# Optimization experiments

Hardware: AMD Instinct MI355X
Metric: run time of the kernel (lower is better)

## Reference

```python
import jax, jax.numpy as jnp
import numpy as np

TOP_K = 5


def setup_inputs() -> dict:
    key = jax.random.key(0)
    k1, k2 = jax.random.split(key)
    batch, n_attr, feat_dim = 4096, 64000, 512  # 1000 classes x 64 attrs
    image_features = jax.random.normal(k1, (batch, feat_dim), dtype=jnp.float32)
    # raw (unnormalized) attribute concept features, flattened to (n_attr, feat_dim)
    attr_features = jax.random.normal(k2, (n_attr, feat_dim), dtype=jnp.float32)
    return {"image_features": image_features, "attr_features": attr_features}


def reference(image_features, attr_features):
    # __init__: L2-normalize attribute features along feature dim
    attr_norm = attr_features / jnp.linalg.norm(attr_features, axis=-1, keepdims=True)
    # similarities: (batch, n_attr) dense dot-product matrix
    similarities = image_features @ attr_norm.T
    # top-k along attribute dim
    top_scores, top_indices = jax.lax.top_k(similarities, TOP_K)
    # gather selected attribute vectors: (batch, top_k, feat_dim)
    top_attr_features = attr_norm[top_indices]
    return (top_attr_features, top_scores)
```

## Files before the change

### kernel.cpp

```cpp
#include <hip/hip_runtime.h>
#include <float.h>

#define FEAT 512
#define TOPK 5
#define NSEL 16
#define BM 256
#define BN 256
#define BKT 64
#define NKT (FEAT / BKT)
#define ABYTES (BM * BKT)
#define BUFB (2 * ABYTES)
#define NCB 4

typedef __attribute__((ext_vector_type(4))) int i32x4;

__device__ __forceinline__ void gl_lds16(const void* g, void* lds) {
    __builtin_amdgcn_global_load_lds(
        (const __attribute__((address_space(1))) unsigned int*)g,
        (__attribute__((address_space(3))) unsigned int*)lds, 16, 0, 0);
}

__global__ __launch_bounds__(256) void quant_attr(
    const float* __restrict__ in, signed char* __restrict__ q,
    float* __restrict__ inv) {
    const int w = threadIdx.x >> 6, l = threadIdx.x & 63;
    const int row = blockIdx.x * 4 + w;
    const float4* p = reinterpret_cast<const float4*>(in) + (size_t)row * (FEAT / 4);
    const float4 v0 = p[l * 2], v1 = p[l * 2 + 1];
    float ss = v0.x * v0.x + v0.y * v0.y + v0.z * v0.z + v0.w * v0.w +
               v1.x * v1.x + v1.y * v1.y + v1.z * v1.z + v1.w * v1.w;
#pragma unroll
    for (int m = 1; m < 64; m <<= 1) ss += __shfl_xor(ss, m);
    const float iv = 1.0f / sqrtf(fmaxf(ss, 1e-30f));
    const float qs = iv * 300.0f;
    int qv[8];
    qv[0] = __float2int_rn(v0.x * qs); qv[1] = __float2int_rn(v0.y * qs);
    qv[2] = __float2int_rn(v0.z * qs); qv[3] = __float2int_rn(v0.w * qs);
    qv[4] = __float2int_rn(v1.x * qs); qv[5] = __float2int_rn(v1.y * qs);
    qv[6] = __float2int_rn(v1.z * qs); qv[7] = __float2int_rn(v1.w * qs);
#pragma unroll
    for (int j = 0; j < 8; ++j) qv[j] = min(127, max(-127, qv[j]));
    int2 st;
    st.x = (qv[0] & 255) | ((qv[1] & 255) << 8) | ((qv[2] & 255) << 16) |
           ((unsigned)(qv[3] & 255) << 24);
    st.y = (qv[4] & 255) | ((qv[5] & 255) << 8) | ((qv[6] & 255) << 16) |
           ((unsigned)(qv[7] & 255) << 24);
    *reinterpret_cast<int2*>(q + (size_t)row * FEAT + l * 8) = st;
    if (l == 0) inv[row] = iv;
}

__global__ __launch_bounds__(256) void quant_img(
    const float* __restrict__ in, signed char* __restrict__ q) {
    const int w = threadIdx.x >> 6, l = threadIdx.x & 63;
    const int row = blockIdx.x * 4 + w;
    const float4* p = reinterpret_cast<const float4*>(in) + (size_t)row * (FEAT / 4);
    const float4 v0 = p[l * 2], v1 = p[l * 2 + 1];
    float mx = fmaxf(fmaxf(fmaxf(fabsf(v0.x), fabsf(v0.y)), fmaxf(fabsf(v0.z), fabsf(v0.w))),
                     fmaxf(fmaxf(fabsf(v1.x), fabsf(v1.y)), fmaxf(fabsf(v1.z), fabsf(v1.w))));
#pragma unroll
    for (int m = 1; m < 64; m <<= 1) mx = fmaxf(mx, __shfl_xor(mx, m));
    mx = fmaxf(mx, 1e-20f);
    const float qs = 127.0f / mx;
    const int q0 = __float2int_rn(v0.x * qs), q1 = __float2int_rn(v0.y * qs);
    const int q2 = __float2int_rn(v0.z * qs), q3 = __float2int_rn(v0.w * qs);
    const int q4 = __float2int_rn(v1.x * qs), q5 = __float2int_rn(v1.y * qs);
    const int q6 = __float2int_rn(v1.z * qs), q7 = __float2int_rn(v1.w * qs);
    int2 st;
    st.x = (q0 & 255) | ((q1 & 255) << 8) | ((q2 & 255) << 16) | ((unsigned)(q3 & 255) << 24);
    st.y = (q4 & 255) | ((q5 & 255) << 8) | ((q6 & 255) << 16) | ((unsigned)(q7 & 255) << 24);
    *reinterpret_cast<int2*>(q + (size_t)row * FEAT + l * 8) = st;
}

__global__ __launch_bounds__(512, 2) void coarse_kernel(
    const signed char* __restrict__ attrQ, const signed char* __restrict__ imgQ,
    unsigned* __restrict__ cand, int nablk, int niblk) {
    __shared__ __align__(1024) char lds[3][BUFB];
    const int tid = threadIdx.x;

    const int cpx = gridDim.x >> 3;
    const int wg = ((int)blockIdx.x & 7) * cpx + ((int)blockIdx.x >> 3);
    const int ablock = wg / niblk;
    const int iblock = wg % niblk;

    const int w = tid >> 6, l = tid & 63;
    const int wr = w >> 2, wc = w & 3;
    const int lrow = l & 15, lg = l >> 4;

    const int srow = tid >> 2, sg = tid & 3;
    const int ssw = sg ^ ((srow ^ (srow >> 2)) & 3);
    const signed char* asrc = attrQ + (size_t)(ablock * BM + srow) * FEAT + (ssw << 4);
    const signed char* bsrc = imgQ + (size_t)(iblock * BN + srow) * FEAT + (ssw << 4);

    int a_off[8], b_off[4];
#pragma unroll
    for (int m = 0; m < 8; ++m) {
        const int r = wr * 128 + m * 16 + lrow;
        a_off[m] = r * BKT + ((lg ^ ((r ^ (r >> 2)) & 3)) << 4);
    }
#pragma unroll
    for (int n = 0; n < 4; ++n) {
        const int r = wc * 64 + n * 16 + lrow;
        b_off[n] = ABYTES + r * BKT + ((lg ^ ((r ^ (r >> 2)) & 3)) << 4);
    }

    i32x4 acc[8][4];
#pragma unroll
    for (int m = 0; m < 8; ++m)
#pragma unroll
        for (int n = 0; n < 4; ++n) acc[m][n] = (i32x4){0, 0, 0, 0};

#define STAGE(bufi, kt)                                                      \
    {                                                                        \
        char* d_ = &lds[bufi][tid * 16];                                     \
        gl_lds16(asrc + (kt) * BKT, d_);                                     \
        gl_lds16(asrc + (kt) * BKT + (size_t)128 * FEAT, d_ + 8192);         \
        gl_lds16(bsrc + (kt) * BKT, d_ + 16384);                             \
        gl_lds16(bsrc + (kt) * BKT + (size_t)128 * FEAT, d_ + 24576);        \
    }

    STAGE(0, 0);
    int cur = 0, nxt = 1;
#pragma unroll 1
    for (int t = 0; t < NKT; ++t) {
        if (t < NKT - 1) {
            STAGE(nxt, t + 1);
            asm volatile("s_waitcnt vmcnt(4)" ::: "memory");
        } else {
            asm volatile("s_waitcnt vmcnt(0)" ::: "memory");
        }
        __builtin_amdgcn_s_barrier();
        __builtin_amdgcn_sched_barrier(0);
        const char* buf = &lds[cur][0];
        i32x4 bF[4], aF[8];
#pragma unroll
        for (int n = 0; n < 4; ++n)
            bF[n] = *reinterpret_cast<const i32x4*>(buf + b_off[n]);
#pragma unroll
        for (int m = 0; m < 8; ++m)
            aF[m] = *reinterpret_cast<const i32x4*>(buf + a_off[m]);
        __builtin_amdgcn_s_setprio(1);
#pragma unroll
        for (int m = 0; m < 8; ++m)
#pragma unroll
            for (int n = 0; n < 4; ++n)
                acc[m][n] = __builtin_amdgcn_mfma_i32_16x16x64_i8(
                    aF[m], bF[n], acc[m][n], 0, 0, 0);
        __builtin_amdgcn_s_setprio(0);
        cur = (cur == 2) ? 0 : cur + 1;
        nxt = (nxt == 2) ? 0 : nxt + 1;
    }
#undef STAGE

    unsigned m1[4] = {0u, 0u, 0u, 0u}, m2[4] = {0u, 0u, 0u, 0u};
#pragma unroll
    for (int m = 0; m < 8; ++m)
#pragma unroll
        for (int r = 0; r < 4; ++r) {
            const int rowl = wr * 128 + m * 16 + lg * 4 + r;
            const unsigned idxc = 2047u - (unsigned)rowl;
#pragma unroll
            for (int n = 0; n < 4; ++n) {
                const unsigned p =
                    (((unsigned)(acc[m][n][r] + (1 << 23)) << 8) & 0xFFFFF800u) | idxc;
                m2[n] = max(m2[n], min(m1[n], p));
                m1[n] = max(m1[n], p);
            }
        }

    unsigned* scratch = reinterpret_cast<unsigned*>(&lds[0][0]);
#pragma unroll
    for (int n = 0; n < 4; ++n) {
        scratch[(w * 64 + l) * 8 + n * 2] = m1[n];
        scratch[(w * 64 + l) * 8 + n * 2 + 1] = m2[n];
    }
    __syncthreads();

    if (tid < BN) {
        const int wc2 = tid >> 6, cw = tid & 63;
        const int n = cw >> 4, lr = cw & 15;
        unsigned best[NCB] = {0u, 0u, 0u, 0u};
#pragma unroll
        for (int wr2 = 0; wr2 < 2; ++wr2)
#pragma unroll
            for (int lg2 = 0; lg2 < 4; ++lg2)
#pragma unroll
                for (int k = 0; k < 2; ++k) {
                    const unsigned p =
                        scratch[((wr2 * 4 + wc2) * 64 + lg2 * 16 + lr) * 8 + n * 2 + k];
                    if (p > best[NCB - 1]) {
                        best[NCB - 1] = p;
#pragma unroll
                        for (int x = NCB - 1; x > 0; --x)
                            if (best[x] > best[x - 1]) {
                                const unsigned t_ = best[x];
                                best[x] = best[x - 1]; best[x - 1] = t_;
                            }
                    }
                }
        const size_t base = ((size_t)(iblock * BN + tid) * nablk + ablock) * NCB;
#pragma unroll
        for (int j = 0; j < NCB; ++j) cand[base + j] = best[j];
    }
}

__global__ __launch_bounds__(64) void select16_kernel(
    const unsigned* __restrict__ cand, int* __restrict__ sel, int nablk) {
    const int row = blockIdx.x;
    const int l = threadIdx.x;
    const int ncand = nablk * NCB;
    const unsigned* cr = cand + (size_t)row * ncand;
    unsigned p[16]; int c[16];
#pragma unroll
    for (int j = 0; j < 16; ++j) {
        const int slot = l * 16 + j;
        if (slot < ncand) {
            const unsigned v = cr[slot];
            p[j] = v;
            c[j] = (slot / NCB) * BM + (2047 - (int)(v & 0x7FFu));
        } else { p[j] = 0u; c[j] = 0x7fffffff; }
    }
    int* out = sel + (size_t)row * NSEL;
    for (int r = 0; r < NSEL; ++r) {
        unsigned bp = 0u; int bc = 0x7fffffff;
#pragma unroll
        for (int j = 0; j < 16; ++j)
            if (p[j] > bp || (p[j] == bp && c[j] < bc)) { bp = p[j]; bc = c[j]; }
#pragma unroll
        for (int m = 1; m < 64; m <<= 1) {
            const unsigned op = __shfl_xor(bp, m);
            const int oc = __shfl_xor(bc, m);
            if (op > bp || (op == bp && oc < bc)) { bp = op; bc = oc; }
        }
        if (l == 0) out[r] = bc;
#pragma unroll
        for (int j = 0; j < 16; ++j)
            if (p[j] == bp && c[j] == bc) { p[j] = 0u; c[j] = 0x7fffffff; }
    }
}

__global__ __launch_bounds__(256) void rescore_kernel(
    const float* __restrict__ img, const float* __restrict__ attr,
    const float* __restrict__ inv, const int* __restrict__ sel,
    float* __restrict__ out_scores, int* __restrict__ final_i) {
    __shared__ float s_sc[NSEL];
    const int row = blockIdx.x;
    const int w = threadIdx.x >> 6, l = threadIdx.x & 63;
    const float4* ip = reinterpret_cast<const float4*>(img) + (size_t)row * (FEAT / 4);
    const float4 a0 = ip[l * 2], a1 = ip[l * 2 + 1];
#pragma unroll
    for (int q = 0; q < 4; ++q) {
        const int slot = w * 4 + q;
        const int ci = sel[(size_t)row * NSEL + slot];
        const float4* ap = reinterpret_cast<const float4*>(attr) + (size_t)ci * (FEAT / 4);
        const float4 b0 = ap[l * 2], b1 = ap[l * 2 + 1];
        float d = a0.x * b0.x + a0.y * b0.y + a0.z * b0.z + a0.w * b0.w +
                  a1.x * b1.x + a1.y * b1.y + a1.z * b1.z + a1.w * b1.w;
#pragma unroll
        for (int m = 1; m < 64; m <<= 1) d += __shfl_xor(d, m);
        if (l == 0) s_sc[slot] = d * inv[ci];
    }
    __syncthreads();
    if (threadIdx.x == 0) {
        float ts[TOPK]; int ti[TOPK];
#pragma unroll
        for (int j = 0; j < TOPK; ++j) { ts[j] = -FLT_MAX; ti[j] = 0x7fffffff; }
        for (int e = 0; e < NSEL; ++e) {
            const float sv = s_sc[e];
            const int iv = sel[(size_t)row * NSEL + e];
            if (sv > ts[4] || (sv == ts[4] && iv < ti[4])) {
                ts[4] = sv; ti[4] = iv;
#pragma unroll
                for (int x = 4; x > 0; --x)
                    if (ts[x] > ts[x - 1] || (ts[x] == ts[x - 1] && ti[x] < ti[x - 1])) {
                        const float tf = ts[x]; ts[x] = ts[x - 1]; ts[x - 1] = tf;
                        const int td = ti[x]; ti[x] = ti[x - 1]; ti[x - 1] = td;
                    }
            }
        }
#pragma unroll
        for (int j = 0; j < TOPK; ++j) {
            out_scores[(size_t)row * TOPK + j] = ts[j];
            final_i[(size_t)row * TOPK + j] = ti[j];
        }
    }
}

__global__ __launch_bounds__(128) void gather_kernel(
    const float* __restrict__ attr, const float* __restrict__ inv,
    const int* __restrict__ final_i, float* __restrict__ out0) {
    const int pair = blockIdx.x;
    const int fi = final_i[pair];
    const float sc = inv[fi];
    const float4 v =
        reinterpret_cast<const float4*>(attr)[(size_t)fi * (FEAT / 4) + threadIdx.x];
    float4 o;
    o.x = v.x * sc; o.y = v.y * sc; o.z = v.z * sc; o.w = v.w * sc;
    reinterpret_cast<float4*>(out0)[(size_t)pair * (FEAT / 4) + threadIdx.x] = o;
}

extern "C" void kernel_launch(void* const* d_in, const int* in_sizes, int n_in,
                              void* d_out, int out_size, void* d_ws, size_t ws_size,
                              hipStream_t stream) {
    const float* img = (const float*)d_in[0];
    const float* attr = (const float*)d_in[1];
    const int batch = in_sizes[0] / FEAT;
    const int nattr = in_sizes[1] / FEAT;
    const int nablk = nattr / BM;
    const int niblk = batch / BN;

    char* ws = (char*)d_ws;
    signed char* attrQ = (signed char*)ws; ws += (size_t)nattr * FEAT;
    signed char* imgQ = (signed char*)ws;  ws += (size_t)batch * FEAT;
    float* inv = (float*)ws;               ws += (size_t)nattr * 4;
    unsigned* cand = (unsigned*)ws;        ws += (size_t)batch * nablk * NCB * 4;
    int* sel = (int*)ws;                   ws += (size_t)batch * NSEL * 4;
    int* final_i = (int*)ws;               ws += (size_t)batch * TOPK * 4;

    float* out0 = (float*)d_out;
    float* out_scores = out0 + (size_t)batch * TOPK * FEAT;

    quant_attr<<<nattr / 4, 256, 0, stream>>>(attr, attrQ, inv);
    quant_img<<<batch / 4, 256, 0, stream>>>(img, imgQ);
    coarse_kernel<<<nablk * niblk, 512, 0, stream>>>(attrQ, imgQ, cand, nablk, niblk);
    select16_kernel<<<batch, 64, 0, stream>>>(cand, sel, nablk);
    rescore_kernel<<<batch, 256, 0, stream>>>(img, attr, inv, sel, out_scores, final_i);
    gather_kernel<<<batch * TOPK, 128, 0, stream>>>(attr, inv, final_i, out0);
}
```

Measured before the change: 282.2 us.

## Deepen GEMM K-loop pipeline with two-ahead prefetch and register double-buffering

The int8 MFMA main loop now issues global-to-LDS loads two tiles ahead across three LDS buffers instead of one ahead. It also loads the next tile's A/B fragments from LDS into a second register set while the MFMAs run on the current set. The loop is fully unrolled with hand-placed waitcnt and barriers. The aim is to hide both global-load latency and LDS-read latency behind matrix-core work. The cost is roughly twice the fragment registers, which could lower occupancy or cause spilling, plus a larger unrolled loop body.

```diff
diff --git a/kernel.cpp b/kernel.cpp
--- a/kernel.cpp
+++ b/kernel.cpp
@@ -109,6 +109,8 @@
 #pragma unroll
         for (int n = 0; n < 4; ++n) acc[m][n] = (i32x4){0, 0, 0, 0};
 
+    i32x4 fAa[8], fAb[4], fBa[8], fBb[4];
+
 #define STAGE(bufi, kt)                                                      \
     {                                                                        \
         char* d_ = &lds[bufi][tid * 16];                                     \
@@ -118,38 +120,56 @@
         gl_lds16(bsrc + (kt) * BKT + (size_t)128 * FEAT, d_ + 24576);        \
     }
 
-    STAGE(0, 0);
-    int cur = 0, nxt = 1;
-#pragma unroll 1
+#define READF(da, db, bufi)                                                  \
+    {                                                                        \
+        const char* buf_ = &lds[bufi][0];                                    \
+        _Pragma("unroll")                                                    \
+        for (int n_ = 0; n_ < 4; ++n_)                                       \
+            db[n_] = *reinterpret_cast<const i32x4*>(buf_ + b_off[n_]);      \
+        _Pragma("unroll")                                                    \
+        for (int m_ = 0; m_ < 8; ++m_)                                       \
+            da[m_] = *reinterpret_cast<const i32x4*>(buf_ + a_off[m_]);      \
+    }
+
+#define MM(fa, fb)                                                           \
+    {                                                                        \
+        __builtin_amdgcn_s_setprio(1);                                       \
+        _Pragma("unroll")                                                    \
+        for (int m_ = 0; m_ < 8; ++m_)                                       \
+            _Pragma("unroll")                                                \
+            for (int n_ = 0; n_ < 4; ++n_)                                   \
+                acc[m_][n_] = __builtin_amdgcn_mfma_i32_16x16x64_i8(         \
+                    fa[m_], fb[n_], acc[m_][n_], 0, 0, 0);                   \
+        __builtin_amdgcn_s_setprio(0);                                       \
+    }
+
+    STAGE(0, 0); STAGE(1, 1); STAGE(2, 2);
+    asm volatile("s_waitcnt vmcnt(8)" ::: "memory");
+    __builtin_amdgcn_s_barrier();
+    __builtin_amdgcn_sched_barrier(0);
+    READF(fAa, fAb, 0);
+
+#pragma unroll
     for (int t = 0; t < NKT; ++t) {
-        if (t < NKT - 1) {
-            STAGE(nxt, t + 1);
+        asm volatile("s_waitcnt lgkmcnt(0)" ::: "memory");
+        if (t <= 5) {
             asm volatile("s_waitcnt vmcnt(4)" ::: "memory");
         } else {
             asm volatile("s_waitcnt vmcnt(0)" ::: "memory");
         }
         __builtin_amdgcn_s_barrier();
         __builtin_amdgcn_sched_barrier(0);
-        const char* buf = &lds[cur][0];
-        i32x4 bF[4], aF[8];
-#pragma unroll
-        for (int n = 0; n < 4; ++n)
-            bF[n] = *reinterpret_cast<const i32x4*>(buf + b_off[n]);
-#pragma unroll
-        for (int m = 0; m < 8; ++m)
-            aF[m] = *reinterpret_cast<const i32x4*>(buf + a_off[m]);
-        __builtin_amdgcn_s_setprio(1);
-#pragma unroll
-        for (int m = 0; m < 8; ++m)
-#pragma unroll
-            for (int n = 0; n < 4; ++n)
-                acc[m][n] = __builtin_amdgcn_mfma_i32_16x16x64_i8(
-                    aF[m], bF[n], acc[m][n], 0, 0, 0);
-        __builtin_amdgcn_s_setprio(0);
-        cur = (cur == 2) ? 0 : cur + 1;
-        nxt = (nxt == 2) ? 0 : nxt + 1;
+        if (t + 3 < NKT) STAGE(t % 3, t + 3);
+        if (t + 1 < NKT) {
+            if (t & 1) { READF(fAa, fAb, (t + 1) % 3); }
+            else       { READF(fBa, fBb, (t + 1) % 3); }
+        }
+        __builtin_amdgcn_sched_barrier(0);
+        if (t & 1) { MM(fBa, fBb); } else { MM(fAa, fAb); }
     }
 #undef STAGE
+#undef READF
+#undef MM
 
     unsigned m1[4] = {0u, 0u, 0u, 0u}, m2[4] = {0u, 0u, 0u, 0u};
 #pragma unroll
```

New measurement: 284.3 us. About the same (+0.8%).

## Shrink coarse GEMM tile to 256x128 with 4 waves and double buffering

Applied to the files above, without the earlier changes.

The int8 coarse similarity kernel now uses 256-row by 128-column tiles, computed by 4 waves instead of 8, with each wave keeping its 128x64 register sub-tile. The LDS pipeline goes from three buffers to two, and an extra barrier after the MFMA block guards buffer reuse. The aim is to cut LDS footprint and launch twice as many smaller workgroups for better occupancy and scheduling flexibility. The cost is more global traffic for the attribute operand, which is reloaded for every column tile, plus an extra synchronization per k-step.

```diff
diff --git a/kernel.cpp b/kernel.cpp
--- a/kernel.cpp
+++ b/kernel.cpp
@@ -5,11 +5,12 @@
 #define TOPK 5
 #define NSEL 16
 #define BM 256
-#define BN 256
+#define BN 128
 #define BKT 64
 #define NKT (FEAT / BKT)
-#define ABYTES (BM * BKT)
-#define BUFB (2 * ABYTES)
+#define A_BYTES (BM * BKT)
+#define B_BYTES (BN * BKT)
+#define BUFB (A_BYTES + B_BYTES)
 #define NCB 4
 
 typedef __attribute__((ext_vector_type(4))) int i32x4;
@@ -71,10 +72,10 @@
     *reinterpret_cast<int2*>(q + (size_t)row * FEAT + l * 8) = st;
 }
 
-__global__ __launch_bounds__(512, 2) void coarse_kernel(
+__global__ __launch_bounds__(256, 2) void coarse_kernel(
     const signed char* __restrict__ attrQ, const signed char* __restrict__ imgQ,
     unsigned* __restrict__ cand, int nablk, int niblk) {
-    __shared__ __align__(1024) char lds[3][BUFB];
+    __shared__ __align__(1024) char lds[2][BUFB];
     const int tid = threadIdx.x;
 
     const int cpx = gridDim.x >> 3;
@@ -83,7 +84,7 @@
     const int iblock = wg % niblk;
 
     const int w = tid >> 6, l = tid & 63;
-    const int wr = w >> 2, wc = w & 3;
+    const int wr = w >> 1, wc = w & 1;
     const int lrow = l & 15, lg = l >> 4;
 
     const int srow = tid >> 2, sg = tid & 3;
@@ -100,7 +101,7 @@
 #pragma unroll
     for (int n = 0; n < 4; ++n) {
         const int r = wc * 64 + n * 16 + lrow;
-        b_off[n] = ABYTES + r * BKT + ((lg ^ ((r ^ (r >> 2)) & 3)) << 4);
+        b_off[n] = A_BYTES + r * BKT + ((lg ^ ((r ^ (r >> 2)) & 3)) << 4);
     }
 
     i32x4 acc[8][4];
@@ -112,26 +113,30 @@
 #define STAGE(bufi, kt)                                                      \
     {                                                                        \
         char* d_ = &lds[bufi][tid * 16];                                     \
-        gl_lds16(asrc + (kt) * BKT, d_);                                     \
-        gl_lds16(asrc + (kt) * BKT + (size_t)128 * FEAT, d_ + 8192);         \
-        gl_lds16(bsrc + (kt) * BKT, d_ + 16384);                             \
-        gl_lds16(bsrc + (kt) * BKT + (size_t)128 * FEAT, d_ + 24576);        \
+        _Pragma("unroll")                                                    \
+        for (int i_ = 0; i_ < 4; ++i_)                                       \
+            gl_lds16(asrc + (kt) * BKT + (size_t)i_ * 64 * FEAT,             \
+                     d_ + i_ * 4096);                                        \
+        _Pragma("unroll")                                                    \
+        for (int j_ = 0; j_ < 2; ++j_)                                       \
+            gl_lds16(bsrc + (kt) * BKT + (size_t)j_ * 64 * FEAT,             \
+                     d_ + A_BYTES + j_ * 4096);                              \
     }
 
     STAGE(0, 0);
-    int cur = 0, nxt = 1;
+    int cur = 0;
 #pragma unroll 1
     for (int t = 0; t < NKT; ++t) {
         if (t < NKT - 1) {
-            STAGE(nxt, t + 1);
-            asm volatile("s_waitcnt vmcnt(4)" ::: "memory");
+            STAGE(cur ^ 1, t + 1);
+            asm volatile("s_waitcnt vmcnt(6)" ::: "memory");
         } else {
             asm volatile("s_waitcnt vmcnt(0)" ::: "memory");
         }
         __builtin_amdgcn_s_barrier();
         __builtin_amdgcn_sched_barrier(0);
         const char* buf = &lds[cur][0];
-        i32x4 bF[4], aF[8];
+        i32x4 aF[8], bF[4];
 #pragma unroll
         for (int n = 0; n < 4; ++n)
             bF[n] = *reinterpret_cast<const i32x4*>(buf + b_off[n]);
@@ -146,8 +151,9 @@
                 acc[m][n] = __builtin_amdgcn_mfma_i32_16x16x64_i8(
                     aF[m], bF[n], acc[m][n], 0, 0, 0);
         __builtin_amdgcn_s_setprio(0);
-        cur = (cur == 2) ? 0 : cur + 1;
-        nxt = (nxt == 2) ? 0 : nxt + 1;
+        __builtin_amdgcn_sched_barrier(0);
+        __builtin_amdgcn_s_barrier();
+        cur ^= 1;
     }
 #undef STAGE
 
@@ -186,7 +192,7 @@
 #pragma unroll
                 for (int k = 0; k < 2; ++k) {
                     const unsigned p =
-                        scratch[((wr2 * 4 + wc2) * 64 + lg2 * 16 + lr) * 8 + n * 2 + k];
+                        scratch[((wr2 * 2 + wc2) * 64 + lg2 * 16 + lr) * 8 + n * 2 + k];
                     if (p > best[NCB - 1]) {
                         best[NCB - 1] = p;
 #pragma unroll
@@ -321,7 +327,7 @@
 
     quant_attr<<<nattr / 4, 256, 0, stream>>>(attr, attrQ, inv);
     quant_img<<<batch / 4, 256, 0, stream>>>(img, imgQ);
-    coarse_kernel<<<nablk * niblk, 512, 0, stream>>>(attrQ, imgQ, cand, nablk, niblk);
+    coarse_kernel<<<nablk * niblk, 256, 0, stream>>>(attrQ, imgQ, cand, nablk, niblk);
     select16_kernel<<<batch, 64, 0, stream>>>(cand, sel, nablk);
     rescore_kernel<<<batch, 256, 0, stream>>>(img, attr, inv, sel, out_scores, final_i);
     gather_kernel<<<batch * TOPK, 128, 0, stream>>>(attr, inv, final_i, out0);
```

New measurement: 284.5 us (median of 2 runs). No clear change (+0.8%).
